# Kernel optimization log

Hardware: AMD Instinct MI355X
Metric: run time of the kernel (lower is better)

The kernel has to match this reference:

```python
import jax, jax.numpy as jnp
import numpy as np

B, C, H, W = 64, 64, 128, 128
K = 7
PAD = 3


def setup_inputs() -> dict:
    key = jax.random.key(0)
    kx, kw, kb = jax.random.split(key, 3)
    scale = (C * K) ** (-0.5)
    x = jax.random.normal(kx, (B, C, H, W), dtype=jnp.float32)
    w = jax.random.normal(kw, (C, K, K), dtype=jnp.float32) * scale
    bias = jax.random.normal(kb, (1,), dtype=jnp.float32) * scale
    return {"x": x, "w": w, "bias": bias}


def reference(x, w, bias):
    # Single-output-channel 2D cross-correlation (sums over all input channels),
    # with zero padding PAD on both spatial dims, stride 1.
    # Matches the torch module's per-pixel loop: out[b, oh, ow] =
    #   sum_{c,dh,dw} x_pad[b, c, oh+dh, ow+dw] * w[c, dh, dw] + bias
    out = jax.lax.conv_general_dilated(
        x,                      # (B, C, H, W)
        w[None, :, :, :],       # (O=1, C, K, K)
        window_strides=(1, 1),
        padding=[(PAD, PAD), (PAD, PAD)],
        dimension_numbers=("NCHW", "OIHW", "NCHW"),
    )
    return out[:, 0] + bias  # (B, H_out, W_out)
```

## Files before the change

kernel.cpp:

```cpp
#include <hip/hip_runtime.h>
#include <stdint.h>


typedef short bf16x8 __attribute__((ext_vector_type(8)));
typedef float f32x4 __attribute__((ext_vector_type(4)));

#define HB    16
#define NR    22
#define XS    36
#define XCOLS 134
#define XBUF  (XCOLS * XS)
#define RROW  132
#define RING_DW (8 * 7 * RROW)

__device__ __forceinline__ uint32_t pk2bf(float a, float b) {
    uint32_t ua = __builtin_bit_cast(uint32_t, a);
    uint32_t ub = __builtin_bit_cast(uint32_t, b);
    ua += 0x7FFFu + ((ua >> 16) & 1u);
    ub += 0x7FFFu + ((ub >> 16) & 1u);
    return (ua >> 16) | (ub & 0xFFFF0000u);
}

__global__ __launch_bounds__(256, 2)
void conv_mfma(const float* __restrict__ x, const float* __restrict__ w,
               const float* __restrict__ bias, float* __restrict__ out) {
    __shared__ uint32_t xlds[2][XBUF];
    __shared__ float    ring[RING_DW];

    const int tid  = threadIdx.x;
    const int lane = tid & 63;
    const int wv   = tid >> 6;
    const int b    = blockIdx.x >> 3;
    const int h0   = (blockIdx.x & 7) * HB;
    const int r0   = h0 - 3;

    const int nl = lane & 15;
    const int q  = lane >> 4;

    for (int i = tid; i < 2 * 6 * XS; i += 256) {
        int bi   = i / (6 * XS);
        int rem  = i - bi * (6 * XS);
        int colh = rem / XS;
        int dwi  = rem - colh * XS;
        int col  = (colh < 3) ? colh : (128 + colh);
        xlds[bi][col * XS + dwi] = 0u;
    }

    bf16x8 Bf[14];
#pragma unroll
    for (int kk = 0; kk < 14; kk++) {
        const int dw = kk >> 1, c0 = (kk & 1) * 32;
        bf16x8 f;
#pragma unroll
        for (int j = 0; j < 8; j++) {
            float v = (nl < 7) ? w[(c0 + 8 * q + j) * 49 + nl * 7 + dw] : 0.f;
            uint32_t u = __builtin_bit_cast(uint32_t, v);
            u += 0x7FFFu + ((u >> 16) & 1u);
            f[j] = (short)(u >> 16);
        }
        Bf[kk] = f;
    }

    const int colq = tid & 31;
    const int cb   = (tid >> 5) * 8;
    const float4* xp = (const float4*)x + (size_t)b * 262144;

    float4 pre[8];
    {
        const bool v = ((unsigned)r0 < 128u);
        const int base = r0 * 32 + colq;
#pragma unroll
        for (int i = 0; i < 8; i++) {
            float4 g = {0.f, 0.f, 0.f, 0.f};
            if (v) g = xp[(cb + i) * 4096 + base];
            pre[i] = g;
        }
    }

    const float bv = bias[0];
    const int m = nl;

#pragma unroll 1
    for (int it = 0; it < NR; it++) {
        const int r = r0 + it;
        uint32_t* buf = xlds[it & 1];

        float fa[8][4];
#pragma unroll
        for (int i = 0; i < 8; i++) {
            fa[i][0] = pre[i].x; fa[i][1] = pre[i].y;
            fa[i][2] = pre[i].z; fa[i][3] = pre[i].w;
        }
#pragma unroll
        for (int j = 0; j < 4; j++) {
            uint4 u;
            u.x = pk2bf(fa[0][j], fa[1][j]);
            u.y = pk2bf(fa[2][j], fa[3][j]);
            u.z = pk2bf(fa[4][j], fa[5][j]);
            u.w = pk2bf(fa[6][j], fa[7][j]);
            *(uint4*)&buf[(4 * colq + j + 3) * XS + (cb >> 1)] = u;
        }
        __syncthreads();

        if (it + 1 < NR) {
            const int rn = r + 1;
            const bool v = ((unsigned)rn < 128u);
            const int base = rn * 32 + colq;
#pragma unroll
            for (int i = 0; i < 8; i++) {
                float4 g = {0.f, 0.f, 0.f, 0.f};
                if (v) g = xp[(cb + i) * 4096 + base];
                pre[i] = g;
            }
        }

        f32x4 acc0 = {0.f, 0.f, 0.f, 0.f};
        f32x4 acc1 = {0.f, 0.f, 0.f, 0.f};
#pragma unroll
        for (int kk = 0; kk < 14; kk++) {
            const int dw  = kk >> 1;
            const int c0h = (kk & 1) * 16;
            const uint32_t* a0 = &buf[(32 * wv + m + dw) * XS + c0h + 4 * q];
            uint4 A0 = *(const uint4*)a0;
            uint4 A1 = *(const uint4*)(a0 + 16 * XS);
            acc0 = __builtin_amdgcn_mfma_f32_16x16x32_bf16(
                       __builtin_bit_cast(bf16x8, A0), Bf[kk], acc0, 0, 0, 0);
            acc1 = __builtin_amdgcn_mfma_f32_16x16x32_bf16(
                       __builtin_bit_cast(bf16x8, A1), Bf[kk], acc1, 0, 0, 0);
        }

        if (nl < 7) {
            const int slot = (r + 8) & 7;
            float* dst = &ring[(slot * 7 + nl) * RROW + 32 * wv + 4 * q];
            *(f32x4*)dst = acc0;
            *(f32x4*)(dst + 16) = acc1;
        }
        __syncthreads();

        const int oh = r - 3;
        if (oh >= h0 && tid < 128) {
            float s = bv;
#pragma unroll
            for (int dh = 0; dh < 7; dh++) {
                const int pr = oh + dh - 3;
                s += ring[(((pr + 8) & 7) * 7 + dh) * RROW + tid];
            }
            out[b * 16384 + oh * 128 + tid] = s;
        }
    }
}

extern "C" void kernel_launch(void* const* d_in, const int* in_sizes, int n_in,
                              void* d_out, int out_size, void* d_ws, size_t ws_size,
                              hipStream_t stream) {
    const float* x    = (const float*)d_in[0];
    const float* w    = (const float*)d_in[1];
    const float* bias = (const float*)d_in[2];
    float* out        = (float*)d_out;

    hipLaunchKernelGGL(conv_mfma, dim3(512), dim3(256), 0, stream, x, w, bias, out);
}
```

Baseline: 379.2 us.

## Software-pipeline row staging and merge barriers into one per iteration

Restructures the main loop so the next row is converted and written to the alternate LDS buffer after the MFMA compute, and the global prefetch runs two rows ahead. This removes one of the two block-wide barriers per iteration, replacing them with a single custom lgkmcnt-wait-plus-barrier. It also remaps threads so eight consecutive threads cover the eight channel groups of one column, which changes the global access and LDS write patterns. Ring slot indexing is simplified to use the iteration counter. The trade-off is a longer register live range for the prefetched data, and reliance on hand-written barrier semantics for correctness.

```diff
diff --git a/kernel.cpp b/kernel.cpp
--- a/kernel.cpp
+++ b/kernel.cpp
@@ -21,9 +21,13 @@
     return (ua >> 16) | (ub & 0xFFFF0000u);
 }
 
+__device__ __forceinline__ void lds_barrier() {
+    asm volatile("s_waitcnt lgkmcnt(0)\n\ts_barrier" ::: "memory");
+}
+
 __global__ __launch_bounds__(256, 2)
-void conv_mfma(const float* __restrict__ x, const float* __restrict__ w,
-               const float* __restrict__ bias, float* __restrict__ out) {
+void conv_mfma_v4(const float* __restrict__ x, const float* __restrict__ w,
+                  const float* __restrict__ bias, float* __restrict__ out) {
     __shared__ uint32_t xlds[2][XBUF];
     __shared__ float    ring[RING_DW];
 
@@ -61,8 +65,8 @@
         Bf[kk] = f;
     }
 
-    const int colq = tid & 31;
-    const int cb   = (tid >> 5) * 8;
+    const int cgrp = tid & 7;
+    const int colq = tid >> 3;
     const float4* xp = (const float4*)x + (size_t)b * 262144;
 
     float4 pre[8];
@@ -72,19 +76,12 @@
 #pragma unroll
         for (int i = 0; i < 8; i++) {
             float4 g = {0.f, 0.f, 0.f, 0.f};
-            if (v) g = xp[(cb + i) * 4096 + base];
+            if (v) g = xp[(8 * cgrp + i) * 4096 + base];
             pre[i] = g;
         }
     }
 
-    const float bv = bias[0];
-    const int m = nl;
-
-#pragma unroll 1
-    for (int it = 0; it < NR; it++) {
-        const int r = r0 + it;
-        uint32_t* buf = xlds[it & 1];
-
+    {
         float fa[8][4];
 #pragma unroll
         for (int i = 0; i < 8; i++) {
@@ -98,21 +95,27 @@
             u.y = pk2bf(fa[2][j], fa[3][j]);
             u.z = pk2bf(fa[4][j], fa[5][j]);
             u.w = pk2bf(fa[6][j], fa[7][j]);
-            *(uint4*)&buf[(4 * colq + j + 3) * XS + (cb >> 1)] = u;
+            *(uint4*)&xlds[0][(4 * colq + j + 3) * XS + 4 * cgrp] = u;
         }
-        __syncthreads();
+        const int rn = r0 + 1;
+        const bool v = ((unsigned)rn < 128u);
+        const int base = rn * 32 + colq;
+#pragma unroll
+        for (int i = 0; i < 8; i++) {
+            float4 g = {0.f, 0.f, 0.f, 0.f};
+            if (v) g = xp[(8 * cgrp + i) * 4096 + base];
+            pre[i] = g;
+        }
+    }
+    lds_barrier();
 
-        if (it + 1 < NR) {
-            const int rn = r + 1;
-            const bool v = ((unsigned)rn < 128u);
-            const int base = rn * 32 + colq;
-#pragma unroll
-            for (int i = 0; i < 8; i++) {
-                float4 g = {0.f, 0.f, 0.f, 0.f};
-                if (v) g = xp[(cb + i) * 4096 + base];
-                pre[i] = g;
-            }
-        }
+    const float bv = bias[0];
+    const int m = nl;
+
+#pragma unroll 1
+    for (int it = 0; it < NR; it++) {
+        const int r = r0 + it;
+        const uint32_t* buf = xlds[it & 1];
 
         f32x4 acc0 = {0.f, 0.f, 0.f, 0.f};
         f32x4 acc1 = {0.f, 0.f, 0.f, 0.f};
@@ -130,21 +133,49 @@
         }
 
         if (nl < 7) {
-            const int slot = (r + 8) & 7;
-            float* dst = &ring[(slot * 7 + nl) * RROW + 32 * wv + 4 * q];
+            float* dst = &ring[((it & 7) * 7 + nl) * RROW + 32 * wv + 4 * q];
             *(f32x4*)dst = acc0;
             *(f32x4*)(dst + 16) = acc1;
         }
-        __syncthreads();
 
-        const int oh = r - 3;
-        if (oh >= h0 && tid < 128) {
+        if (it + 1 < NR) {
+            float fa[8][4];
+#pragma unroll
+            for (int i = 0; i < 8; i++) {
+                fa[i][0] = pre[i].x; fa[i][1] = pre[i].y;
+                fa[i][2] = pre[i].z; fa[i][3] = pre[i].w;
+            }
+            uint32_t* nbuf = xlds[(it + 1) & 1];
+#pragma unroll
+            for (int j = 0; j < 4; j++) {
+                uint4 u;
+                u.x = pk2bf(fa[0][j], fa[1][j]);
+                u.y = pk2bf(fa[2][j], fa[3][j]);
+                u.z = pk2bf(fa[4][j], fa[5][j]);
+                u.w = pk2bf(fa[6][j], fa[7][j]);
+                *(uint4*)&nbuf[(4 * colq + j + 3) * XS + 4 * cgrp] = u;
+            }
+            if (it + 2 < NR) {
+                const int rn = r + 2;
+                const bool v = ((unsigned)rn < 128u);
+                const int base = rn * 32 + colq;
+#pragma unroll
+                for (int i = 0; i < 8; i++) {
+                    float4 g = {0.f, 0.f, 0.f, 0.f};
+                    if (v) g = xp[(8 * cgrp + i) * 4096 + base];
+                    pre[i] = g;
+                }
+            }
+        }
+
+        lds_barrier();
+
+        if (it >= 6 && tid < 128) {
+            const int oh = r - 3;
             float s = bv;
 #pragma unroll
-            for (int dh = 0; dh < 7; dh++) {
-                const int pr = oh + dh - 3;
-                s += ring[(((pr + 8) & 7) * 7 + dh) * RROW + tid];
-            }
+            for (int dh = 0; dh < 7; dh++)
+                s += ring[(((it - 6 + dh) & 7) * 7 + dh) * RROW + tid];
             out[b * 16384 + oh * 128 + tid] = s;
         }
     }
@@ -158,5 +189,5 @@
     const float* bias = (const float*)d_in[2];
     float* out        = (float*)d_out;
 
-    hipLaunchKernelGGL(conv_mfma, dim3(512), dim3(256), 0, stream, x, w, bias, out);
+    hipLaunchKernelGGL(conv_mfma_v4, dim3(512), dim3(256), 0, stream, x, w, bias, out);
 }
```

New measurement: 381.0 us. No clear change (+0.5%).

## Split input channels across two blocks, process two rows per barrier, atomically combine outputs

Applied to the files above, without the earlier changes.

The kernel now splits the 64 input channels into two halves handled by separate blocks, so the grid doubles and a memset plus atomicAdd merges the partial outputs. Each iteration stages two input rows at once, halving the number of barriers, and replaces the 7-slot ring with an in-place accumulator that sums the dh contributions as they arrive. LDS per block shrinks, allowing three blocks per CU. The cost is atomic traffic to global memory, an extra memset launch, and read-modify-write accumulation in LDS.

```diff
diff --git a/kernel.cpp b/kernel.cpp
--- a/kernel.cpp
+++ b/kernel.cpp
@@ -6,12 +6,11 @@
 typedef float f32x4 __attribute__((ext_vector_type(4)));
 
 #define HB    16
-#define NR    22
-#define XS    36
+#define XS    20
 #define XCOLS 134
-#define XBUF  (XCOLS * XS)
-#define RROW  132
-#define RING_DW (8 * 7 * RROW)
+#define XB1   (XCOLS * XS)
+#define AROW  132
+#define NSLOT 8
 
 __device__ __forceinline__ uint32_t pk2bf(float a, float b) {
     uint32_t ua = __builtin_bit_cast(uint32_t, a);
@@ -21,39 +20,48 @@
     return (ua >> 16) | (ub & 0xFFFF0000u);
 }
 
-__global__ __launch_bounds__(256, 2)
-void conv_mfma(const float* __restrict__ x, const float* __restrict__ w,
-               const float* __restrict__ bias, float* __restrict__ out) {
-    __shared__ uint32_t xlds[2][XBUF];
-    __shared__ float    ring[RING_DW];
+__device__ __forceinline__ void lds_barrier() {
+    asm volatile("s_waitcnt lgkmcnt(0)\n\ts_barrier" ::: "memory");
+}
+
+__global__ __launch_bounds__(256, 3)
+void conv_v6(const float* __restrict__ x, const float* __restrict__ w,
+             const float* __restrict__ bias, float* __restrict__ out) {
+    __shared__ uint32_t xlds[2][2 * XB1];
+    __shared__ float    acc[NSLOT * AROW];
 
     const int tid  = threadIdx.x;
     const int lane = tid & 63;
     const int wv   = tid >> 6;
-    const int b    = blockIdx.x >> 3;
-    const int h0   = (blockIdx.x & 7) * HB;
+    const int bx   = blockIdx.x;
+    const int cs   = bx & 1;
+    const int band = (bx >> 1) & 7;
+    const int b    = bx >> 4;
+    const int h0   = band * HB;
     const int r0   = h0 - 3;
 
     const int nl = lane & 15;
     const int q  = lane >> 4;
 
-    for (int i = tid; i < 2 * 6 * XS; i += 256) {
-        int bi   = i / (6 * XS);
-        int rem  = i - bi * (6 * XS);
-        int colh = rem / XS;
-        int dwi  = rem - colh * XS;
+    for (int i = tid; i < NSLOT * AROW; i += 256) acc[i] = 0.f;
+    for (int i = tid; i < 2 * 2 * 6 * XS; i += 256) {
+        int bi   = i / (2 * 6 * XS);
+        int rem  = i - bi * (2 * 6 * XS);
+        int rs   = rem / (6 * XS);
+        int rem2 = rem - rs * (6 * XS);
+        int colh = rem2 / XS;
+        int dwi  = rem2 - colh * XS;
         int col  = (colh < 3) ? colh : (128 + colh);
-        xlds[bi][col * XS + dwi] = 0u;
+        xlds[bi][rs * XB1 + col * XS + dwi] = 0u;
     }
 
-    bf16x8 Bf[14];
+    bf16x8 Bf[7];
 #pragma unroll
-    for (int kk = 0; kk < 14; kk++) {
-        const int dw = kk >> 1, c0 = (kk & 1) * 32;
+    for (int kk = 0; kk < 7; kk++) {
         bf16x8 f;
 #pragma unroll
         for (int j = 0; j < 8; j++) {
-            float v = (nl < 7) ? w[(c0 + 8 * q + j) * 49 + nl * 7 + dw] : 0.f;
+            float v = (nl < 7) ? w[(32 * cs + 8 * q + j) * 49 + nl * 7 + kk] : 0.f;
             uint32_t u = __builtin_bit_cast(uint32_t, v);
             u += 0x7FFFu + ((u >> 16) & 1u);
             f[j] = (short)(u >> 16);
@@ -61,92 +69,118 @@
         Bf[kk] = f;
     }
 
-    const int colq = tid & 31;
-    const int cb   = (tid >> 5) * 8;
-    const float4* xp = (const float4*)x + (size_t)b * 262144;
+    const int cgrp = tid & 3;
+    const int rsel = tid >> 7;
+    const int colq = (tid >> 2) & 31;
+    const float4* xp4 =
+        (const float4*)x + ((size_t)b * 64 + 32 * cs + 8 * cgrp) * 4096;
 
     float4 pre[8];
+
     {
-        const bool v = ((unsigned)r0 < 128u);
-        const int base = r0 * 32 + colq;
+        const int r = r0 + rsel;
+        const bool v = ((unsigned)r < 128u);
+        const int base = r * 32 + colq;
 #pragma unroll
         for (int i = 0; i < 8; i++) {
             float4 g = {0.f, 0.f, 0.f, 0.f};
-            if (v) g = xp[(cb + i) * 4096 + base];
+            if (v) g = xp4[i * 4096 + base];
+            pre[i] = g;
+        }
+#pragma unroll
+        for (int j = 0; j < 4; j++) {
+            float c0 = (&pre[0].x)[j], c1 = (&pre[1].x)[j], c2 = (&pre[2].x)[j],
+                  c3 = (&pre[3].x)[j], c4 = (&pre[4].x)[j], c5 = (&pre[5].x)[j],
+                  c6 = (&pre[6].x)[j], c7 = (&pre[7].x)[j];
+            uint4 u;
+            u.x = pk2bf(c0, c1); u.y = pk2bf(c2, c3);
+            u.z = pk2bf(c4, c5); u.w = pk2bf(c6, c7);
+            *(uint4*)&xlds[0][rsel * XB1 + (4 * colq + j + 3) * XS + 4 * cgrp] = u;
+        }
+        const int rn = r0 + 2 + rsel;
+        const bool vn = ((unsigned)rn < 128u);
+        const int basen = rn * 32 + colq;
+#pragma unroll
+        for (int i = 0; i < 8; i++) {
+            float4 g = {0.f, 0.f, 0.f, 0.f};
+            if (vn) g = xp4[i * 4096 + basen];
             pre[i] = g;
         }
     }
+    lds_barrier();
 
-    const float bv = bias[0];
-    const int m = nl;
+    const float bv = (cs == 0) ? bias[0] : 0.f;
 
 #pragma unroll 1
-    for (int it = 0; it < NR; it++) {
-        const int r = r0 + it;
-        uint32_t* buf = xlds[it & 1];
+    for (int k = 0; k < 11; k++) {
+        const uint32_t* buf = xlds[k & 1];
 
-        float fa[8][4];
 #pragma unroll
-        for (int i = 0; i < 8; i++) {
-            fa[i][0] = pre[i].x; fa[i][1] = pre[i].y;
-            fa[i][2] = pre[i].z; fa[i][3] = pre[i].w;
-        }
+        for (int sub = 0; sub < 2; sub++) {
+            const int r = r0 + 2 * k + sub;
+            f32x4 a0 = {0.f, 0.f, 0.f, 0.f};
+            f32x4 a1 = {0.f, 0.f, 0.f, 0.f};
+            const uint32_t* rowbuf = buf + sub * XB1;
 #pragma unroll
-        for (int j = 0; j < 4; j++) {
-            uint4 u;
-            u.x = pk2bf(fa[0][j], fa[1][j]);
-            u.y = pk2bf(fa[2][j], fa[3][j]);
-            u.z = pk2bf(fa[4][j], fa[5][j]);
-            u.w = pk2bf(fa[6][j], fa[7][j]);
-            *(uint4*)&buf[(4 * colq + j + 3) * XS + (cb >> 1)] = u;
-        }
-        __syncthreads();
-
-        if (it + 1 < NR) {
-            const int rn = r + 1;
-            const bool v = ((unsigned)rn < 128u);
-            const int base = rn * 32 + colq;
+            for (int kk = 0; kk < 7; kk++) {
+                const uint32_t* ap = &rowbuf[(32 * wv + nl + kk) * XS + 4 * q];
+                uint4 A0 = *(const uint4*)ap;
+                uint4 A1 = *(const uint4*)(ap + 16 * XS);
+                a0 = __builtin_amdgcn_mfma_f32_16x16x32_bf16(
+                         __builtin_bit_cast(bf16x8, A0), Bf[kk], a0, 0, 0, 0);
+                a1 = __builtin_amdgcn_mfma_f32_16x16x32_bf16(
+                         __builtin_bit_cast(bf16x8, A1), Bf[kk], a1, 0, 0, 0);
+            }
+            if (nl < 7) {
+                const int oh = r + 3 - nl;
+                if ((unsigned)(oh - h0) < (unsigned)HB) {
+                    const int s = oh & 7;
+                    float* p0 = &acc[s * AROW + 32 * wv + 4 * q];
+                    f32x4 c0 = *(f32x4*)p0;
+                    f32x4 c1 = *(f32x4*)(p0 + 16);
 #pragma unroll
-            for (int i = 0; i < 8; i++) {
-                float4 g = {0.f, 0.f, 0.f, 0.f};
-                if (v) g = xp[(cb + i) * 4096 + base];
-                pre[i] = g;
+                    for (int j = 0; j < 4; j++) { c0[j] += a0[j]; c1[j] += a1[j]; }
+                    *(f32x4*)p0 = c0;
+                    *(f32x4*)(p0 + 16) = c1;
+                }
             }
         }
 
-        f32x4 acc0 = {0.f, 0.f, 0.f, 0.f};
-        f32x4 acc1 = {0.f, 0.f, 0.f, 0.f};
-#pragma unroll
-        for (int kk = 0; kk < 14; kk++) {
-            const int dw  = kk >> 1;
-            const int c0h = (kk & 1) * 16;
-            const uint32_t* a0 = &buf[(32 * wv + m + dw) * XS + c0h + 4 * q];
-            uint4 A0 = *(const uint4*)a0;
-            uint4 A1 = *(const uint4*)(a0 + 16 * XS);
-            acc0 = __builtin_amdgcn_mfma_f32_16x16x32_bf16(
-                       __builtin_bit_cast(bf16x8, A0), Bf[kk], acc0, 0, 0, 0);
-            acc1 = __builtin_amdgcn_mfma_f32_16x16x32_bf16(
-                       __builtin_bit_cast(bf16x8, A1), Bf[kk], acc1, 0, 0, 0);
+        if (k >= 3) {
+            const int oh  = r0 + 2 * k - 3 + (lane >> 5);
+            const int col = 32 * wv + (lane & 31);
+            float* ap = &acc[(oh & 7) * AROW + col];
+            float v = *ap + bv;
+            *ap = 0.f;
+            atomicAdd(&out[(size_t)b * 16384 + oh * 128 + col], v);
         }
 
-        if (nl < 7) {
-            const int slot = (r + 8) & 7;
-            float* dst = &ring[(slot * 7 + nl) * RROW + 32 * wv + 4 * q];
-            *(f32x4*)dst = acc0;
-            *(f32x4*)(dst + 16) = acc1;
+        if (k <= 9) {
+            uint32_t* nbuf = xlds[(k + 1) & 1];
+#pragma unroll
+            for (int j = 0; j < 4; j++) {
+                float c0 = (&pre[0].x)[j], c1 = (&pre[1].x)[j], c2 = (&pre[2].x)[j],
+                      c3 = (&pre[3].x)[j], c4 = (&pre[4].x)[j], c5 = (&pre[5].x)[j],
+                      c6 = (&pre[6].x)[j], c7 = (&pre[7].x)[j];
+                uint4 u;
+                u.x = pk2bf(c0, c1); u.y = pk2bf(c2, c3);
+                u.z = pk2bf(c4, c5); u.w = pk2bf(c6, c7);
+                *(uint4*)&nbuf[rsel * XB1 + (4 * colq + j + 3) * XS + 4 * cgrp] = u;
+            }
+            if (k <= 8) {
+                const int rn = r0 + 2 * (k + 2) + rsel;
+                const bool vn = ((unsigned)rn < 128u);
+                const int basen = rn * 32 + colq;
+#pragma unroll
+                for (int i = 0; i < 8; i++) {
+                    float4 g = {0.f, 0.f, 0.f, 0.f};
+                    if (vn) g = xp4[i * 4096 + basen];
+                    pre[i] = g;
+                }
+            }
         }
-        __syncthreads();
 
-        const int oh = r - 3;
-        if (oh >= h0 && tid < 128) {
-            float s = bv;
-#pragma unroll
-            for (int dh = 0; dh < 7; dh++) {
-                const int pr = oh + dh - 3;
-                s += ring[(((pr + 8) & 7) * 7 + dh) * RROW + tid];
-            }
-            out[b * 16384 + oh * 128 + tid] = s;
-        }
+        lds_barrier();
     }
 }
 
@@ -158,5 +192,6 @@
     const float* bias = (const float*)d_in[2];
     float* out        = (float*)d_out;
 
-    hipLaunchKernelGGL(conv_mfma, dim3(512), dim3(256), 0, stream, x, w, bias, out);
+    hipMemsetAsync(d_out, 0, (size_t)out_size * sizeof(float), stream);
+    hipLaunchKernelGGL(conv_v6, dim3(1024), dim3(256), 0, stream, x, w, bias, out);
 }
```

Measured after the change: 373.9 us. Within noise of the previous version (-1.4%).
